# Kernel tuning notes

Measured on AMD Instinct MI355X. Metric: run time of the kernel, lower is better.

The kernel has to match this reference:

```python
import jax, jax.numpy as jnp
import numpy as np

N = 100000
E = 1600000
D_IN = 128
D_HID = 128
D_OUT = 64
NUM_LAYERS = 4


def setup_inputs() -> dict:
    key = jax.random.key(0)
    ks = jax.random.split(key, 12)
    features = jax.random.normal(ks[0], (N, D_IN), dtype=jnp.float32)
    edge_index = jax.random.randint(ks[1], (2, E), 0, N, dtype=jnp.int64)
    def glorot(k, shape):
        fan_in, fan_out = shape
        s = jnp.sqrt(6.0 / (fan_in + fan_out)).astype(jnp.float32)
        return jax.random.uniform(k, shape, jnp.float32, -s, s)
    W0 = glorot(ks[2], (D_IN, D_HID)); b0 = jnp.zeros((D_HID,), jnp.float32)
    W1 = glorot(ks[3], (D_HID, D_HID)); b1 = jnp.zeros((D_HID,), jnp.float32)
    W2 = glorot(ks[4], (D_HID, D_HID)); b2 = jnp.zeros((D_HID,), jnp.float32)
    W3 = glorot(ks[5], (D_HID, D_OUT)); b3 = jnp.zeros((D_OUT,), jnp.float32)
    return {"features": features, "edge_index": edge_index,
            "W0": W0, "b0": b0, "W1": W1, "b1": b1,
            "W2": W2, "b2": b2, "W3": W3, "b3": b3}


def _degree_norms(edge_index):
    src, dst = edge_index[0], edge_index[1]
    ones = jnp.ones((src.shape[0],), jnp.float32)
    out_deg = jax.ops.segment_sum(ones, src, num_segments=N)
    in_deg = jax.ops.segment_sum(ones, dst, num_segments=N)
    norm_src = jnp.where(out_deg > 0, jax.lax.rsqrt(jnp.maximum(out_deg, 1.0)), 0.0)
    norm_dst = jnp.where(in_deg > 0, jax.lax.rsqrt(jnp.maximum(in_deg, 1.0)), 0.0)
    return norm_src, norm_dst


def _graph_conv(x, W, b, src, dst, norm_src, norm_dst, act):
    # linear transform first (aggregation is linear, order-equivalent)
    h = x @ W                                   # [N, d_out]
    h = h * norm_src[:, None]                   # symmetric norm, src side
    msg = jnp.take(h, src, axis=0)              # gather  [E, d_out]
    agg = jax.ops.segment_sum(msg, dst, num_segments=N)  # scatter-add [N, d_out]
    agg = agg * norm_dst[:, None]               # symmetric norm, dst side
    agg = agg + b
    if act:
        agg = jnp.tanh(agg)
    return agg


def reference(features, edge_index, W0, b0, W1, b1, W2, b2, W3, b3):
    src, dst = edge_index[0], edge_index[1]
    norm_src, norm_dst = _degree_norms(edge_index)
    x = _graph_conv(features, W0, b0, src, dst, norm_src, norm_dst, act=True)
    x = _graph_conv(x, W1, b1, src, dst, norm_src, norm_dst, act=True)
    x = _graph_conv(x, W2, b2, src, dst, norm_src, norm_dst, act=True)
    x = _graph_conv(x, W3, b3, src, dst, norm_src, norm_dst, act=False)  # last layer: no activation
    return x
```

## Files before the change

### kernel.cpp

```cpp
#include <hip/hip_runtime.h>
#include <cmath>

typedef __attribute__((ext_vector_type(8))) short bf16x8;
typedef __attribute__((ext_vector_type(8))) _Float16 f16x8;
typedef __attribute__((ext_vector_type(4))) float f32x4;

__device__ inline unsigned short f2bf_rne(float f) {
    unsigned int u = __float_as_uint(f);
    unsigned int r = (u + 0x7FFFu + ((u >> 16) & 1u)) >> 16;
    return (unsigned short)r;
}
__device__ inline float bf2f(unsigned short h) {
    return __uint_as_float(((unsigned int)h) << 16);
}

__device__ inline float fast_tanh(float x) {
    float e = x * 2.8853900817779268f;
    e = fminf(fmaxf(e, -126.f), 126.f);
    float t = __builtin_amdgcn_exp2f(e);
    return (t - 1.0f) * __builtin_amdgcn_rcpf(t + 1.0f);
}


constexpr int CB = 256;

__global__ __launch_bounds__(256) void k_bucket_hist(const int* __restrict__ src,
                                                     const int* __restrict__ dst,
                                                     int* __restrict__ gH,
                                                     int E, int K, int scanN, int chunk) {
    extern __shared__ int lds[];
    int* hd = lds; int* hs = lds + K;
    for (int i = threadIdx.x; i < 2 * K; i += 256) lds[i] = 0;
    __syncthreads();
    int lo = blockIdx.x * chunk;
    int hi = lo + chunk; if (hi > E) hi = E;
    for (int i = lo + threadIdx.x; i < hi; i += 256) {
        atomicAdd(&hd[dst[i] >> 6], 1);
        atomicAdd(&hs[src[i] >> 6], 1);
    }
    __syncthreads();
    for (int k = threadIdx.x; k < K; k += 256) {
        gH[(size_t)k * CB + blockIdx.x] = hd[k];
        gH[(size_t)(scanN + k * CB) + blockIdx.x] = hs[k];
    }
}

__global__ __launch_bounds__(256) void k_bucket_scatter(const int* __restrict__ src,
                                                        const int* __restrict__ dst,
                                                        const int* __restrict__ gHS,
                                                        int* __restrict__ sortedAll,
                                                        int E, int K, int scanN, int chunk) {
    extern __shared__ int lds[];
    int* bd = lds; int* bs = lds + K;
    for (int k = threadIdx.x; k < K; k += 256) {
        bd[k] = gHS[(size_t)k * CB + blockIdx.x];
        bs[k] = gHS[(size_t)(scanN + k * CB) + blockIdx.x];
    }
    __syncthreads();
    int lo = blockIdx.x * chunk;
    int hi = lo + chunk; if (hi > E) hi = E;
    for (int i = lo + threadIdx.x; i < hi; i += 256) {
        int d = dst[i], s = src[i];
        int pd = atomicAdd(&bd[d >> 6], 1);
        sortedAll[pd] = ((d & 63) << 17) | s;
        int ps = atomicAdd(&bs[s >> 6], 1);
        sortedAll[ps] = s;
    }
}

__global__ __launch_bounds__(256) void k_fine(const int* __restrict__ sortedAll,
                                              const int* __restrict__ gHS,
                                              int* __restrict__ rowptr,
                                              int* __restrict__ colidx,
                                              float* __restrict__ nsrc,
                                              float* __restrict__ ndst,
                                              int E, int K, int scanN, int N) {
    __shared__ int cnt[64], excl[64], rank[64];
    int kb = blockIdx.x;
    bool isDst = kb < K;
    int k = isDst ? kb : kb - K;
    int bstart, bend;
    if (isDst) {
        bstart = gHS[(size_t)k * CB];
        bend = (k + 1 < K) ? gHS[(size_t)(k + 1) * CB] : E;
    } else {
        bstart = gHS[(size_t)(scanN + k * CB)];
        bend = (k + 1 < K) ? gHS[(size_t)(scanN + (k + 1) * CB)] : 2 * E;
    }
    if (threadIdx.x < 64) { cnt[threadIdx.x] = 0; rank[threadIdx.x] = 0; }
    __syncthreads();
    if (isDst) {
        for (int i = bstart + threadIdx.x; i < bend; i += 256)
            atomicAdd(&cnt[sortedAll[i] >> 17], 1);
    } else {
        for (int i = bstart + threadIdx.x; i < bend; i += 256)
            atomicAdd(&cnt[sortedAll[i] & 63], 1);
    }
    __syncthreads();
    if (isDst) {
        if (threadIdx.x == 0) {
            int r = 0;
            for (int j = 0; j < 64; j++) { excl[j] = r; r += cnt[j]; }
        }
        __syncthreads();
        int node0 = k << 6;
        if (threadIdx.x < 64) {
            int node = node0 + threadIdx.x;
            if (node < N) {
                rowptr[node] = bstart + excl[threadIdx.x];
                int c = cnt[threadIdx.x];
                ndst[node] = c > 0 ? rsqrtf((float)c) : 0.f;
            }
        }
        if (k == 0 && threadIdx.x == 0) rowptr[N] = E;
        for (int i = bstart + threadIdx.x; i < bend; i += 256) {
            int v = sortedAll[i];
            int n = v >> 17;
            int r = atomicAdd(&rank[n], 1);
            colidx[bstart + excl[n] + r] = v & 0x1FFFF;
        }
    } else {
        int node = (k << 6) + threadIdx.x;
        if (threadIdx.x < 64 && node < N) {
            int c = cnt[threadIdx.x];
            nsrc[node] = c > 0 ? rsqrtf((float)c) : 0.f;
        }
    }
}

__global__ void k_prepW_all(const float* __restrict__ W0, const float* __restrict__ W1,
                            const float* __restrict__ W2, const float* __restrict__ W3,
                            unsigned short* __restrict__ h0, unsigned short* __restrict__ l0,
                            unsigned short* __restrict__ h1, unsigned short* __restrict__ l1,
                            unsigned short* __restrict__ h2, unsigned short* __restrict__ l2,
                            unsigned short* __restrict__ h3, unsigned short* __restrict__ l3) {
    int i = blockIdx.x * 256 + threadIdx.x;
    const float* W; unsigned short* wh; unsigned short* wl; int N; int base;
    if      (i < 16384) { W = W0; wh = h0; wl = l0; N = 128; base = i; }
    else if (i < 32768) { W = W1; wh = h1; wl = l1; N = 128; base = i - 16384; }
    else if (i < 49152) { W = W2; wh = h2; wl = l2; N = 128; base = i - 32768; }
    else if (i < 57344) { W = W3; wh = h3; wl = l3; N = 64;  base = i - 49152; }
    else return;
    int n = base >> 7, k = base & 127;
    float w = W[k * N + n];
    unsigned short hb = f2bf_rne(w);
    unsigned short lb = f2bf_rne(w - bf2f(hb));
    wh[base] = hb; wl[base] = lb;
}


constexpr int SCAN_TILE = 2048;

__global__ __launch_bounds__(256) void k_scan_partial(const int* __restrict__ deg,
                                                      int* __restrict__ tilesum, int n) {
    __shared__ int red[256];
    int base = blockIdx.x * SCAN_TILE;
    int s = 0;
    for (int i = threadIdx.x; i < SCAN_TILE; i += 256) {
        int idx = base + i;
        if (idx < n) s += deg[idx];
    }
    red[threadIdx.x] = s;
    __syncthreads();
    for (int off = 128; off > 0; off >>= 1) {
        if (threadIdx.x < off) red[threadIdx.x] += red[threadIdx.x + off];
        __syncthreads();
    }
    if (threadIdx.x == 0) tilesum[blockIdx.x] = red[0];
}

__global__ void k_scan_tiles(int* __restrict__ tilesum, int* __restrict__ outArr,
                             int numTiles, int n) {
    if (threadIdx.x == 0 && blockIdx.x == 0) {
        int acc = 0;
        for (int i = 0; i < numTiles; i++) { int v = tilesum[i]; tilesum[i] = acc; acc += v; }
        outArr[n] = acc;
    }
}

__global__ __launch_bounds__(256) void k_scan_final(const int* __restrict__ deg,
                                                    const int* __restrict__ tilesum,
                                                    int* __restrict__ outArr, int n) {
    __shared__ int red[256];
    int base = blockIdx.x * SCAN_TILE;
    int lo = base + threadIdx.x * 8;
    int v[8]; int s = 0;
#pragma unroll
    for (int j = 0; j < 8; j++) {
        int idx = lo + j;
        v[j] = (idx < n) ? deg[idx] : 0;
        s += v[j];
    }
    red[threadIdx.x] = s;
    __syncthreads();
    for (int off = 1; off < 256; off <<= 1) {
        int x = red[threadIdx.x];
        int add = (threadIdx.x >= off) ? red[threadIdx.x - off] : 0;
        __syncthreads();
        red[threadIdx.x] = x + add;
        __syncthreads();
    }
    int excl = tilesum[blockIdx.x] + (threadIdx.x ? red[threadIdx.x - 1] : 0);
#pragma unroll
    for (int j = 0; j < 8; j++) {
        int idx = lo + j;
        if (idx < n) outArr[idx] = excl;
        excl += v[j];
    }
}


template <int DOUT, int SRC>
__global__ __launch_bounds__(256) void k_gemm_hyb(
        const float* __restrict__ xf,
        const unsigned short* __restrict__ xhi, const unsigned short* __restrict__ xlo,
        const unsigned short* __restrict__ wth, const unsigned short* __restrict__ wtl,
        const float* __restrict__ nsrc, _Float16* __restrict__ h, int nrows) {
    constexpr int NT = DOUT / 16;
    constexpr int LDK = 72;
    __shared__ unsigned short Bh[DOUT * LDK], Bl[DOUT * LDK];

    int tid = threadIdx.x;
    int lane = tid & 63;
    int wv = tid >> 6;
    int quad = lane >> 4, l16 = lane & 15;
    int r0 = blockIdx.x * 64 + wv * 16;
    int rowA = r0 + l16; if (rowA >= nrows) rowA = nrows - 1;

    if (blockIdx.x == 0 && tid < DOUT / 8) {
        float4 z = {0.f, 0.f, 0.f, 0.f};
        *(float4*)((char*)h + ((size_t)nrows * DOUT + tid * 8) * 2) = z;
    }

    f32x4 acc[NT];
#pragma unroll
    for (int nt = 0; nt < NT; nt++) acc[nt] = (f32x4){0.f, 0.f, 0.f, 0.f};

    for (int kh = 0; kh < 2; kh++) {
        if (kh) __syncthreads();
        for (int i = tid; i < DOUT * 16; i += 256) {
            int n = i >> 4, kb = i & 15;
            int koff = kh * 64 + kb * 4;
            *(ushort4*)&Bh[n * LDK + kb * 4] = *(const ushort4*)&wth[n * 128 + koff];
            *(ushort4*)&Bl[n * LDK + kb * 4] = *(const ushort4*)&wtl[n * 128 + koff];
        }
        __syncthreads();

#pragma unroll
        for (int kq = 0; kq < 2; kq++) {
            int koA = kh * 64 + kq * 32 + quad * 8;
            int koB = kq * 32 + quad * 8;
            bf16x8 ah, al;
            if (SRC == 0) {
                const float* xp = &xf[(size_t)rowA * 128 + koA];
                float4 x0 = *(const float4*)xp;
                float4 x1 = *(const float4*)(xp + 4);
                union { bf16x8 v; unsigned short u[8]; } H, L;
                float xs[8] = {x0.x, x0.y, x0.z, x0.w, x1.x, x1.y, x1.z, x1.w};
#pragma unroll
                for (int j = 0; j < 8; j++) {
                    H.u[j] = f2bf_rne(xs[j]);
                    L.u[j] = f2bf_rne(xs[j] - bf2f(H.u[j]));
                }
                ah = H.v; al = L.v;
            } else {
                ah = *(const bf16x8*)&xhi[(size_t)rowA * 128 + koA];
                al = *(const bf16x8*)&xlo[(size_t)rowA * 128 + koA];
            }
#pragma unroll
            for (int nt = 0; nt < NT; nt++) {
                int n = nt * 16 + l16;
                bf16x8 bh = *(const bf16x8*)&Bh[n * LDK + koB];
                bf16x8 bl = *(const bf16x8*)&Bl[n * LDK + koB];
                acc[nt] = __builtin_amdgcn_mfma_f32_16x16x32_bf16(ah, bh, acc[nt], 0, 0, 0);
                acc[nt] = __builtin_amdgcn_mfma_f32_16x16x32_bf16(ah, bl, acc[nt], 0, 0, 0);
                acc[nt] = __builtin_amdgcn_mfma_f32_16x16x32_bf16(al, bh, acc[nt], 0, 0, 0);
            }
        }
    }

#pragma unroll
    for (int r = 0; r < 4; r++) {
        int row = r0 + quad * 4 + r;
        if (row < nrows) {
            float nm = nsrc[row];
#pragma unroll
            for (int nt = 0; nt < NT; nt++)
                h[(size_t)row * DOUT + nt * 16 + l16] = (_Float16)(acc[nt][r] * nm);
        }
    }
}


template <int D, int MODE>
__global__ __launch_bounds__(256) void k_aggregate(const _Float16* __restrict__ h,
                                                   const int* __restrict__ rowptr,
                                                   const int* __restrict__ colidx,
                                                   const float* __restrict__ ndst,
                                                   const float* __restrict__ bias,
                                                   float* __restrict__ out,
                                                   unsigned short* __restrict__ ohi,
                                                   unsigned short* __restrict__ olo,
                                                   int n) {
    constexpr int FB = D / 8;
    constexpr int GN = 64 / FB;
    constexpr int EU = 4;
    int wid  = (blockIdx.x * 256 + threadIdx.x) >> 6;
    int lane = threadIdx.x & 63;
    int fb = lane & (FB - 1);
    int g  = lane / FB;
    int waveCount = gridDim.x * 4;

    for (int nbase = wid * GN; nbase < n; nbase += waveCount * GN) {
        int node = nbase + g;
        bool vn = node < n;
        int beg = vn ? rowptr[node] : 0;
        int end = vn ? rowptr[node + 1] : 0;
        int m = end - beg;

        int mmax = m;
#pragma unroll
        for (int off = FB; off < 64; off <<= 1) {
            int t = __shfl_xor(mmax, off);
            mmax = mmax > t ? mmax : t;
        }

        float acc[8];
#pragma unroll
        for (int k = 0; k < 8; k++) acc[k] = 0.f;

        int cv = 0;
        for (int j0 = 0; j0 < mmax; j0 += EU) {
            if ((j0 & (FB - 1)) == 0) {
                int idx = beg + j0 + fb;
                cv = colidx[idx < end ? idx : 0];
            }
            int s[EU];
#pragma unroll
            for (int u = 0; u < EU; u++) {
                int j = j0 + u;
                int sv = __shfl(cv, g * FB + (j & (FB - 1)));
                s[u] = j < m ? sv : n;
            }
            f16x8 v[EU];
#pragma unroll
            for (int u = 0; u < EU; u++)
                v[u] = *(const f16x8*)&h[(size_t)s[u] * D + fb * 8];
#pragma unroll
            for (int u = 0; u < EU; u++) {
#pragma unroll
                for (int k = 0; k < 8; k++)
                    acc[k] += (float)v[u][k];
            }
        }

        if (vn) {
            float nd = ndst[node];
            float bv[8];
            *(float4*)&bv[0] = ((const float4*)bias)[fb * 2];
            *(float4*)&bv[4] = ((const float4*)bias)[fb * 2 + 1];
            float vv[8];
#pragma unroll
            for (int k = 0; k < 8; k++) vv[k] = acc[k] * nd + bv[k];
            if (MODE == 1) {
                union { bf16x8 v; unsigned short u[8]; } H, L;
#pragma unroll
                for (int k = 0; k < 8; k++) {
                    float t = fast_tanh(vv[k]);
                    H.u[k] = f2bf_rne(t);
                    L.u[k] = f2bf_rne(t - bf2f(H.u[k]));
                }
                *(bf16x8*)&ohi[(size_t)node * D + fb * 8] = H.v;
                *(bf16x8*)&olo[(size_t)node * D + fb * 8] = L.v;
            } else {
                *(float4*)&out[(size_t)node * D + fb * 8] = *(float4*)&vv[0];
                *(float4*)&out[(size_t)node * D + fb * 8 + 4] = *(float4*)&vv[4];
            }
        }
    }
}


extern "C" void kernel_launch(void* const* d_in, const int* in_sizes, int n_in,
                              void* d_out, int out_size, void* d_ws, size_t ws_size,
                              hipStream_t stream) {
    const float* features = (const float*)d_in[0];
    const int* edges      = (const int*)d_in[1];
    const float* W0 = (const float*)d_in[2]; const float* b0 = (const float*)d_in[3];
    const float* W1 = (const float*)d_in[4]; const float* b1 = (const float*)d_in[5];
    const float* W2 = (const float*)d_in[6]; const float* b2 = (const float*)d_in[7];
    const float* W3 = (const float*)d_in[8]; const float* b3 = (const float*)d_in[9];
    float* out = (float*)d_out;

    const int N = in_sizes[0] / 128;
    const int E = in_sizes[1] / 2;
    const int* src = edges;
    const int* dst = edges + E;
    const int K = (N + 63) >> 6;
    const int chunk = (E + CB - 1) / CB;
    const int scanN = K * CB;
    const int n2 = 2 * scanN;
    const int numTiles = (n2 + SCAN_TILE - 1) / SCAN_TILE;
    const size_t dynLds = (size_t)2 * K * sizeof(int);

    char* p = (char*)d_ws;
    _Float16* bufH         = (_Float16*)p;       p += (size_t)N * 128 * 4;
    unsigned short* xhi    = (unsigned short*)p; p += (size_t)(N + 1) * 128 * 2;
    unsigned short* xlo    = (unsigned short*)p; p += (size_t)(N + 1) * 128 * 2;
    int*   rowptr = (int*)p;   p += (((size_t)(N + 1) * 4 + 15) / 16) * 16;
    int*   colidx = (int*)p;   p += (size_t)E * 4;
    float* nsrc   = (float*)p; p += (size_t)N * 4;
    float* ndst   = (float*)p; p += (size_t)N * 4;
    int*   tilesum= (int*)p;   p += (((size_t)(numTiles + 1) * 4 + 15) / 16) * 16;
    unsigned short* wt0h = (unsigned short*)p; p += 16384 * 2;
    unsigned short* wt0l = (unsigned short*)p; p += 16384 * 2;
    unsigned short* wt1h = (unsigned short*)p; p += 16384 * 2;
    unsigned short* wt1l = (unsigned short*)p; p += 16384 * 2;
    unsigned short* wt2h = (unsigned short*)p; p += 16384 * 2;
    unsigned short* wt2l = (unsigned short*)p; p += 16384 * 2;
    unsigned short* wt3h = (unsigned short*)p; p += 8192 * 2;
    unsigned short* wt3l = (unsigned short*)p; p += 8192 * 2;

    char* q = (char*)xhi;
    int* sortedAll = (int*)q; q += (size_t)2 * E * 4;
    int* gH        = (int*)q; q += (size_t)n2 * 4;
    int* gHS       = (int*)q; q += (size_t)(n2 + 1) * 4;

    k_prepW_all<<<224, 256, 0, stream>>>(W0, W1, W2, W3, wt0h, wt0l, wt1h, wt1l,
                                         wt2h, wt2l, wt3h, wt3l);
    k_bucket_hist<<<CB, 256, dynLds, stream>>>(src, dst, gH, E, K, scanN, chunk);
    k_scan_partial<<<numTiles, 256, 0, stream>>>(gH, tilesum, n2);
    k_scan_tiles<<<1, 64, 0, stream>>>(tilesum, gHS, numTiles, n2);
    k_scan_final<<<numTiles, 256, 0, stream>>>(gH, tilesum, gHS, n2);
    k_bucket_scatter<<<CB, 256, dynLds, stream>>>(src, dst, gHS, sortedAll, E, K, scanN, chunk);
    k_fine<<<2 * K, 256, 0, stream>>>(sortedAll, gHS, rowptr, colidx, nsrc, ndst, E, K, scanN, N);

    int gblk = (N + 63) / 64;
    int ablk128 = (N + 15) / 16;
    int ablk64  = (N + 31) / 32;
    k_gemm_hyb<128, 0><<<gblk, 256, 0, stream>>>(features, nullptr, nullptr, wt0h, wt0l, nsrc, bufH, N);
    k_aggregate<128, 1><<<ablk128, 256, 0, stream>>>(bufH, rowptr, colidx, ndst, b0, nullptr, xhi, xlo, N);
    k_gemm_hyb<128, 1><<<gblk, 256, 0, stream>>>(nullptr, xhi, xlo, wt1h, wt1l, nsrc, bufH, N);
    k_aggregate<128, 1><<<ablk128, 256, 0, stream>>>(bufH, rowptr, colidx, ndst, b1, nullptr, xhi, xlo, N);
    k_gemm_hyb<128, 1><<<gblk, 256, 0, stream>>>(nullptr, xhi, xlo, wt2h, wt2l, nsrc, bufH, N);
    k_aggregate<128, 1><<<ablk128, 256, 0, stream>>>(bufH, rowptr, colidx, ndst, b2, nullptr, xhi, xlo, N);
    k_gemm_hyb<64, 1><<<gblk, 256, 0, stream>>>(nullptr, xhi, xlo, wt3h, wt3l, nsrc, bufH, N);
    k_aggregate<64, 0><<<ablk64, 256, 0, stream>>>(bufH, rowptr, colidx, ndst, b3, out, nullptr, nullptr, N);
}
```

Before: 529.3 us.

## Double-buffer neighbor gathers in aggregation loop with 32-bit address math

Restructures the CSR aggregation inner loop into a software pipeline with two register buffers, so the next batch of gathered feature rows is loaded while the current batch is being accumulated. Address computation switches to 32-bit shifted offsets instead of 64-bit size_t multiplies, and accumulation uses fmaf with an opaque 1.0 to control instruction selection. This raises VGPR pressure and assumes the feature buffer stays within a 32-bit byte offset.

```diff
diff --git a/kernel.cpp b/kernel.cpp
--- a/kernel.cpp
+++ b/kernel.cpp
@@ -292,6 +292,32 @@
 }
 
 
+#define LOADB(bidx, vv)                                                        \
+    {                                                                          \
+        int jb = (bidx) * EU;                                                  \
+        if ((jb & (FB - 1)) == 0) {                                            \
+            int idx = beg + jb + fb;                                           \
+            cv = colidx[idx < end ? idx : 0];                                  \
+        }                                                                      \
+        _Pragma("unroll")                                                      \
+        for (int u = 0; u < EU; u++) {                                         \
+            int j = jb + u;                                                    \
+            int sv = __shfl(cv, lbase + (j & (FB - 1)));                       \
+            int s = j < m ? sv : n;                                            \
+            unsigned off = ((unsigned)s << SHS) | (fbo);                       \
+            vv[u] = *(const f16x8*)((const char*)h + off);                     \
+        }                                                                      \
+    }
+
+#define ACCB(vv)                                                               \
+    {                                                                          \
+        _Pragma("unroll")                                                      \
+        for (int u = 0; u < EU; u++)                                           \
+            _Pragma("unroll")                                                  \
+            for (int k = 0; k < 8; k++)                                        \
+                acc[k] = fmaf((float)vv[u][k], one, acc[k]);                   \
+    }
+
 template <int D, int MODE>
 __global__ __launch_bounds__(256) void k_aggregate(const _Float16* __restrict__ h,
                                                    const int* __restrict__ rowptr,
@@ -305,11 +331,17 @@
     constexpr int FB = D / 8;
     constexpr int GN = 64 / FB;
     constexpr int EU = 4;
+    constexpr int SHS = (D == 128) ? 8 : 7;
     int wid  = (blockIdx.x * 256 + threadIdx.x) >> 6;
     int lane = threadIdx.x & 63;
     int fb = lane & (FB - 1);
     int g  = lane / FB;
+    int lbase = lane & ~(FB - 1);
+    unsigned fbo = (unsigned)fb << 4;
     int waveCount = gridDim.x * 4;
+
+    float one = 1.0f;
+    asm volatile("" : "+v"(one));
 
     for (int nbase = wid * GN; nbase < n; nbase += waveCount * GN) {
         int node = nbase + g;
@@ -329,29 +361,26 @@
 #pragma unroll
         for (int k = 0; k < 8; k++) acc[k] = 0.f;
 
-        int cv = 0;
-        for (int j0 = 0; j0 < mmax; j0 += EU) {
-            if ((j0 & (FB - 1)) == 0) {
-                int idx = beg + j0 + fb;
-                cv = colidx[idx < end ? idx : 0];
+        int nb = (mmax + EU - 1) / EU;
+        if (nb > 0) {
+            f16x8 vA[EU], vB[EU];
+            int cv = 0;
+            LOADB(0, vA);
+            int b = 0;
+            while (b + 1 < nb) {
+                LOADB(b + 1, vB);
+                ACCB(vA);
+                b++;
+                if (b + 1 < nb) {
+                    LOADB(b + 1, vA);
+                    ACCB(vB);
+                    b++;
+                } else {
+                    ACCB(vB);
+                    b++;
+                }
             }
-            int s[EU];
-#pragma unroll
-            for (int u = 0; u < EU; u++) {
-                int j = j0 + u;
-                int sv = __shfl(cv, g * FB + (j & (FB - 1)));
-                s[u] = j < m ? sv : n;
-            }
-            f16x8 v[EU];
-#pragma unroll
-            for (int u = 0; u < EU; u++)
-                v[u] = *(const f16x8*)&h[(size_t)s[u] * D + fb * 8];
-#pragma unroll
-            for (int u = 0; u < EU; u++) {
-#pragma unroll
-                for (int k = 0; k < 8; k++)
-                    acc[k] += (float)v[u][k];
-            }
+            if (b < nb) ACCB(vA);
         }
 
         if (vn) {
```

Result: slower. 551.1 us (+4.1%).
